# Performance work log

Measured on AMD Instinct MI355X. Metric: run time of the kernel, lower is better.

Reference implementation:

```python
import jax, jax.numpy as jnp
import numpy as np


def setup_inputs() -> dict:
    key = jax.random.key(0)
    k1, k2 = jax.random.split(key)
    x = jax.random.normal(k1, (16, 512, 64, 64), dtype=jnp.float32)
    # learned scalar (nn.Parameter init zeros; use small random value so output is nontrivial)
    gamma = jax.random.normal(k2, (1,), dtype=jnp.float32) * 0.1
    return {"x": x, "gamma": gamma}


def reference(x, gamma):
    b, c, h, w = x.shape
    q = x.reshape(b, c, h * w)                      # [b, c, hw]
    energy = jnp.einsum('bcn,bdn->bcd', q, q)       # [b, c, c]
    # reverse-max trick: max - energy, then softmax over last dim
    energy_new = jnp.max(energy, axis=-1, keepdims=True) - energy
    attention = jax.nn.softmax(energy_new, axis=-1)  # [b, c, c]
    out = jnp.einsum('bcd,bdn->bcn', attention, q).reshape(b, c, h, w)
    return gamma * out + x
```

## Files before the change

### kernel.cpp

```cpp
#include <hip/hip_runtime.h>


constexpr int Bb = 16;
constexpr int Cc = 512;
constexpr int NN = 4096;

typedef _Float16 half8 __attribute__((ext_vector_type(8)));
typedef _Float16 half4 __attribute__((ext_vector_type(4)));
typedef float float4v __attribute__((ext_vector_type(4)));

__device__ inline void gld_lds16(const _Float16* g, _Float16* l) {
    __builtin_amdgcn_global_load_lds(
        (const __attribute__((address_space(1))) unsigned int*)g,
        (__attribute__((address_space(3))) unsigned int*)l, 16, 0, 0);
}

__global__ __launch_bounds__(256) void prep_kernel(const float* __restrict__ x,
                                                   _Float16* __restrict__ Qh,
                                                   _Float16* __restrict__ QhT) {
    __shared__ float T[64][65];
    const int b = blockIdx.z;
    const int n0 = blockIdx.x * 64;
    const int d0 = blockIdx.y * 64;
    const float* xb = x + ((size_t)b * Cc + d0) * NN + n0;
    const int tid = threadIdx.x;
#pragma unroll
    for (int i = 0; i < 4; ++i) {
        int lin = tid + i * 256;
        int dr = lin >> 4;
        int c4 = (lin & 15) * 4;
        float4 v = *reinterpret_cast<const float4*>(&xb[(size_t)dr * NN + c4]);
        T[dr][c4 + 0] = v.x; T[dr][c4 + 1] = v.y;
        T[dr][c4 + 2] = v.z; T[dr][c4 + 3] = v.w;
    }
    __syncthreads();
#pragma unroll
    for (int i = 0; i < 2; ++i) {
        int widx = tid + i * 256;
        int dr = widx >> 3;
        int cn = widx & 7;
        half8 h;
#pragma unroll
        for (int j = 0; j < 8; ++j) h[j] = (_Float16)T[dr][cn * 8 + j];
        size_t dst = ((size_t)b * Cc + d0 + dr) * NN + n0 + cn * 8;
        *reinterpret_cast<half8*>(&Qh[dst]) = h;
    }
#pragma unroll
    for (int i = 0; i < 2; ++i) {
        int widx = tid + i * 256;
        int nr = widx >> 3;
        int cd = widx & 7;
        half8 h;
#pragma unroll
        for (int j = 0; j < 8; ++j) h[j] = (_Float16)T[cd * 8 + j][nr];
        size_t dst = ((size_t)b * NN + n0 + nr) * Cc + d0 + cd * 8;
        *reinterpret_cast<half8*>(&QhT[dst]) = h;
    }
}

template <int NT, int SPLIT>
__global__ __launch_bounds__(512, 4) void gram_sym(const _Float16* __restrict__ A,
                                                   float* __restrict__ D) {
    __shared__ __align__(16) float gL[128 * 129];
    _Float16* sAB = (_Float16*)gL;
    const int BPB = 10 * SPLIT;
    const int L = blockIdx.x;
    const int t0 = (L & 7) * ((BPB * Bb) >> 3) + (L >> 3);
    const int b = t0 / BPB;
    const int rem = t0 % BPB;
    const int ti = rem / SPLIT;
    const int half = rem % SPLIT;
    const int kBase = half * NT * 64;
    float* Deff = D + (size_t)half * Bb * Cc * Cc;
    int tr, tc;
    if (ti < 4)      { tr = 0; tc = ti; }
    else if (ti < 7) { tr = 1; tc = ti - 3; }
    else if (ti < 9) { tr = 2; tc = ti - 5; }
    else             { tr = 3; tc = 3; }
    const int rowTile = tr * 128;
    const int colTile = tc * 128;

    const _Float16* Ab = A + (size_t)b * Cc * NN;
    const int tid = threadIdx.x;

    float4v acc[4][2];
#pragma unroll
    for (int m = 0; m < 4; ++m)
#pragma unroll
        for (int n = 0; n < 2; ++n) acc[m][n] = (float4v){0.f, 0.f, 0.f, 0.f};

    auto stage = [&](int buf, int kt) {
        const int k0 = kBase + (kt << 6);
        _Float16* sA = sAB + buf * 8192;
        _Float16* sB = sAB + 16384 + buf * 8192;
#pragma unroll
        for (int i = 0; i < 2; ++i) {
            int idx = tid + i * 512;
            int r = idx >> 3;
            int c = idx & 7;
            int cs = (c ^ (r & 7)) << 3;
            gld_lds16(Ab + (size_t)(rowTile + r) * NN + k0 + cs, sA + idx * 8);
            gld_lds16(Ab + (size_t)(colTile + r) * NN + k0 + cs, sB + idx * 8);
        }
    };

    stage(0, 0);
    __syncthreads();

    const int wid = tid >> 6, lane = tid & 63;
    const int wr = wid >> 2, wc = wid & 3;
    const int lr = lane & 15, q = lane >> 4;

    for (int t = 0; t < NT; ++t) {
        if (t + 1 < NT) stage((t + 1) & 1, t + 1);
        const _Float16* cA = sAB + (t & 1) * 8192;
        const _Float16* cB = sAB + 16384 + (t & 1) * 8192;
#pragma unroll
        for (int s = 0; s < 2; ++s) {
            half8 af[4], bf[2];
#pragma unroll
            for (int m = 0; m < 4; ++m) {
                int r = wr * 64 + m * 16 + lr;
                int c = (s * 4 + q) ^ (r & 7);
                af[m] = *reinterpret_cast<const half8*>(&cA[r * 64 + c * 8]);
            }
#pragma unroll
            for (int n = 0; n < 2; ++n) {
                int r = wc * 32 + n * 16 + lr;
                int c = (s * 4 + q) ^ (r & 7);
                bf[n] = *reinterpret_cast<const half8*>(&cB[r * 64 + c * 8]);
            }
#pragma unroll
            for (int m = 0; m < 4; ++m)
#pragma unroll
                for (int n = 0; n < 2; ++n)
                    acc[m][n] = __builtin_amdgcn_mfma_f32_16x16x32_f16(af[m], bf[n], acc[m][n], 0, 0, 0);
        }
        __syncthreads();
    }

    __syncthreads();
#pragma unroll
    for (int m = 0; m < 4; ++m)
#pragma unroll
        for (int n = 0; n < 2; ++n)
#pragma unroll
            for (int e = 0; e < 4; ++e)
                gL[(wr * 64 + m * 16 + q * 4 + e) * 129 + wc * 32 + n * 16 + lr] = acc[m][n][e];
    __syncthreads();

    float* Db = Deff + (size_t)b * Cc * Cc;
#pragma unroll
    for (int k = 0; k < 8; ++k) {
        int c = tid + k * 512;
        int row = c >> 5;
        int col = (c & 31) << 2;
        float4 v = *reinterpret_cast<const float4*>(&gL[row * 129 + col]);
        *reinterpret_cast<float4*>(&Db[(size_t)(rowTile + row) * Cc + colTile + col]) = v;
    }
    if (tr != tc) {
#pragma unroll
        for (int k = 0; k < 8; ++k) {
            int c = tid + k * 512;
            int crow = c >> 5;
            int r4 = (c & 31) << 2;
            float4 v;
            v.x = gL[(r4 + 0) * 129 + crow];
            v.y = gL[(r4 + 1) * 129 + crow];
            v.z = gL[(r4 + 2) * 129 + crow];
            v.w = gL[(r4 + 3) * 129 + crow];
            *reinterpret_cast<float4*>(&Db[(size_t)(colTile + crow) * Cc + rowTile + r4]) = v;
        }
    }
}

template <int RES>
__global__ __launch_bounds__(512, 4) void pv_mfma(const _Float16* __restrict__ A,
                                                  const _Float16* __restrict__ Bp,
                                                  const float* __restrict__ xres,
                                                  const _Float16* __restrict__ Qh,
                                                  const float* __restrict__ gamma,
                                                  float* __restrict__ out) {
    __shared__ __align__(16) _Float16 smem[5 * 8192];
    float* L = (float*)smem;
    const int BPB = 128;
    const int Lb = blockIdx.x;
    const int t0 = (Lb & 7) * ((BPB * Bb) >> 3) + (Lb >> 3);
    const int b = t0 / BPB;
    const int rem = t0 % BPB;
    const int rowTile = (rem & 3) * 128;
    const int colTile = (rem >> 2) * 128;

    const _Float16* Ab = A + (size_t)b * Cc * Cc;
    const _Float16* Bbp = Bp + (size_t)b * NN * Cc;
    const int tid = threadIdx.x;

    float4v acc[4][2];
#pragma unroll
    for (int m = 0; m < 4; ++m)
#pragma unroll
        for (int n = 0; n < 2; ++n) acc[m][n] = (float4v){0.f, 0.f, 0.f, 0.f};

    auto stageA = [&](_Float16* dst, int kt) {
        const int k0 = kt << 6;
#pragma unroll
        for (int i = 0; i < 2; ++i) {
            int idx = tid + i * 512;
            int r = idx >> 3, c = idx & 7;
            int cs = (c ^ (r & 7)) << 3;
            gld_lds16(Ab + (size_t)(rowTile + r) * Cc + k0 + cs, dst + idx * 8);
        }
    };
    auto stageB = [&](_Float16* dst, int kt) {
        const int k0 = kt << 6;
#pragma unroll
        for (int i = 0; i < 2; ++i) {
            int idx = tid + i * 512;
            int r = idx >> 3, c = idx & 7;
            int cs = (c ^ (r & 7)) << 3;
            gld_lds16(Bbp + (size_t)(colTile + r) * Cc + k0 + cs, dst + idx * 8);
        }
    };

    _Float16* sA0 = smem;
    _Float16* sA1 = smem + 8192;
    _Float16* sB_ = smem + 16384;

    stageA(sA0, 0);
    stageB(sB_, 0);
    stageB(sB_ + 8192, 1);

    const int wid = tid >> 6, lane = tid & 63;
    const int wr = wid >> 2, wc = wid & 3;
    const int lr = lane & 15, q = lane >> 4;

#pragma unroll
    for (int t = 0; t < 8; ++t) {
        if (t < 7) asm volatile("s_waitcnt vmcnt(2)" ::: "memory");
        else       asm volatile("s_waitcnt vmcnt(0)" ::: "memory");
        __builtin_amdgcn_s_barrier();
        __builtin_amdgcn_sched_barrier(0);

        const _Float16* cA = (t & 1) ? sA1 : sA0;
        const _Float16* cB = sB_ + (t % 3) * 8192;
        half8 af[2][4], bf[2][2];
#pragma unroll
        for (int s = 0; s < 2; ++s) {
#pragma unroll
            for (int m = 0; m < 4; ++m) {
                int r = wr * 64 + m * 16 + lr;
                int c = (s * 4 + q) ^ (r & 7);
                af[s][m] = *reinterpret_cast<const half8*>(&cA[r * 64 + c * 8]);
            }
#pragma unroll
            for (int n = 0; n < 2; ++n) {
                int r = wc * 32 + n * 16 + lr;
                int c = (s * 4 + q) ^ (r & 7);
                bf[s][n] = *reinterpret_cast<const half8*>(&cB[r * 64 + c * 8]);
            }
        }
        if (t + 1 < 8) stageA((t & 1) ? sA0 : sA1, t + 1);
        if (t + 2 < 8) stageB(sB_ + ((t + 2) % 3) * 8192, t + 2);

        __builtin_amdgcn_s_setprio(1);
#pragma unroll
        for (int s = 0; s < 2; ++s)
#pragma unroll
            for (int m = 0; m < 4; ++m)
#pragma unroll
                for (int n = 0; n < 2; ++n)
                    acc[m][n] = __builtin_amdgcn_mfma_f32_16x16x32_f16(af[s][m], bf[s][n], acc[m][n], 0, 0, 0);
        __builtin_amdgcn_s_setprio(0);
    }

    __syncthreads();
#pragma unroll
    for (int m = 0; m < 4; ++m)
#pragma unroll
        for (int n = 0; n < 2; ++n)
#pragma unroll
            for (int e = 0; e < 4; ++e)
                L[(wr * 64 + m * 16 + q * 4 + e) * 129 + wc * 32 + n * 16 + lr] = acc[m][n][e];
    __syncthreads();

    const float g = gamma[0];
    const size_t base = (size_t)b * Cc * NN;
#pragma unroll
    for (int k = 0; k < 8; ++k) {
        int c = tid + k * 512;
        int row = c >> 5;
        int col = (c & 31) << 2;
        float4 v = *reinterpret_cast<const float4*>(&L[row * 129 + col]);
        size_t o = base + (size_t)(rowTile + row) * NN + colTile + col;
        float4 ov;
        if (RES == 0) {
            float4 xi = *reinterpret_cast<const float4*>(&xres[o]);
            ov.x = fmaf(g, v.x, xi.x); ov.y = fmaf(g, v.y, xi.y);
            ov.z = fmaf(g, v.z, xi.z); ov.w = fmaf(g, v.w, xi.w);
        } else {
            half4 hq = *reinterpret_cast<const half4*>(&Qh[o]);
            ov.x = fmaf(g, v.x, (float)hq[0]); ov.y = fmaf(g, v.y, (float)hq[1]);
            ov.z = fmaf(g, v.z, (float)hq[2]); ov.w = fmaf(g, v.w, (float)hq[3]);
        }
        *reinterpret_cast<float4*>(&out[o]) = ov;
    }
}

template <int HALVES>
__global__ __launch_bounds__(256) void softmax_fp16(const float* __restrict__ eA,
                                                    const float* __restrict__ eB,
                                                    _Float16* __restrict__ attH) {
    const int wave = threadIdx.x >> 6;
    const int lane = threadIdx.x & 63;
    const int row = blockIdx.x * 4 + wave;
    const float* E1 = eA + (size_t)row * Cc;
    float v[8];
    {
        float4 a = *reinterpret_cast<const float4*>(&E1[lane * 8]);
        float4 c = *reinterpret_cast<const float4*>(&E1[lane * 8 + 4]);
        v[0] = a.x; v[1] = a.y; v[2] = a.z; v[3] = a.w;
        v[4] = c.x; v[5] = c.y; v[6] = c.z; v[7] = c.w;
    }
    if (HALVES == 2) {
        const float* E2 = eB + (size_t)row * Cc;
        float4 a = *reinterpret_cast<const float4*>(&E2[lane * 8]);
        float4 c = *reinterpret_cast<const float4*>(&E2[lane * 8 + 4]);
        v[0] += a.x; v[1] += a.y; v[2] += a.z; v[3] += a.w;
        v[4] += c.x; v[5] += c.y; v[6] += c.z; v[7] += c.w;
    }
    float mn = v[0];
#pragma unroll
    for (int i = 1; i < 8; ++i) mn = fminf(mn, v[i]);
#pragma unroll
    for (int off = 32; off; off >>= 1) mn = fminf(mn, __shfl_xor(mn, off, 64));
    float sum = 0.f;
#pragma unroll
    for (int i = 0; i < 8; ++i) {
        v[i] = __expf(mn - v[i]);
        sum += v[i];
    }
#pragma unroll
    for (int off = 32; off; off >>= 1) sum += __shfl_xor(sum, off, 64);
    const float inv = 1.0f / sum;
    half8 h;
#pragma unroll
    for (int i = 0; i < 8; ++i) h[i] = (_Float16)(v[i] * inv);
    *reinterpret_cast<half8*>(&attH[(size_t)row * Cc + lane * 8]) = h;
}

#define TILE 64
#define KT 32
#define PAD 68

__global__ __launch_bounds__(256) void gram_f32(const float* __restrict__ x,
                                                float* __restrict__ energy) {
    __shared__ __align__(16) float As[KT][PAD];
    __shared__ __align__(16) float Bs[KT][PAD];
    const int b = blockIdx.z;
    const int rowTile = blockIdx.y * TILE;
    const int colTile = blockIdx.x * TILE;
    const float* Q = x + (size_t)b * Cc * NN;
    const int t = threadIdx.x;
    const int tx = t & 15;
    const int ty = t >> 4;
    float acc[4][4] = {};
    for (int k0 = 0; k0 < NN; k0 += KT) {
#pragma unroll
        for (int i = 0; i < 8; ++i) {
            int idx = t + i * 256;
            int r = idx >> 5;
            int k = idx & 31;
            As[k][r] = Q[(size_t)(rowTile + r) * NN + k0 + k];
            Bs[k][r] = Q[(size_t)(colTile + r) * NN + k0 + k];
        }
        __syncthreads();
#pragma unroll
        for (int k = 0; k < KT; ++k) {
            float4 a = *reinterpret_cast<const float4*>(&As[k][ty * 4]);
            float4 bq = *reinterpret_cast<const float4*>(&Bs[k][tx * 4]);
            float av[4] = {a.x, a.y, a.z, a.w};
            float bv[4] = {bq.x, bq.y, bq.z, bq.w};
#pragma unroll
            for (int i = 0; i < 4; ++i)
#pragma unroll
                for (int j = 0; j < 4; ++j)
                    acc[i][j] = fmaf(av[i], bv[j], acc[i][j]);
        }
        __syncthreads();
    }
    float* E = energy + (size_t)b * Cc * Cc;
#pragma unroll
    for (int i = 0; i < 4; ++i) {
        const int rowG = rowTile + ty * 4 + i;
        float4 o;
        o.x = acc[i][0]; o.y = acc[i][1]; o.z = acc[i][2]; o.w = acc[i][3];
        *reinterpret_cast<float4*>(&E[(size_t)rowG * Cc + colTile + tx * 4]) = o;
    }
}

__global__ __launch_bounds__(256) void softmax_f32(float* __restrict__ energy) {
    const int wave = threadIdx.x >> 6;
    const int lane = threadIdx.x & 63;
    const int row = blockIdx.x * 4 + wave;
    float* E = energy + (size_t)row * Cc;
    float v[8];
    float mn = 3.4e38f;
#pragma unroll
    for (int i = 0; i < 8; ++i) {
        v[i] = E[lane + 64 * i];
        mn = fminf(mn, v[i]);
    }
#pragma unroll
    for (int off = 32; off; off >>= 1) mn = fminf(mn, __shfl_xor(mn, off, 64));
    float sum = 0.f;
#pragma unroll
    for (int i = 0; i < 8; ++i) {
        v[i] = __expf(mn - v[i]);
        sum += v[i];
    }
#pragma unroll
    for (int off = 32; off; off >>= 1) sum += __shfl_xor(sum, off, 64);
    const float inv = 1.0f / sum;
#pragma unroll
    for (int i = 0; i < 8; ++i) E[lane + 64 * i] = v[i] * inv;
}

__global__ __launch_bounds__(256) void pv_f32(const float* __restrict__ x,
                                              const float* __restrict__ att,
                                              const float* __restrict__ gamma,
                                              float* __restrict__ out) {
    __shared__ __align__(16) float As[KT][PAD];
    __shared__ __align__(16) float Bs[KT][PAD];
    const int b = blockIdx.z;
    const int rowTile = blockIdx.y * TILE;
    const int colTile = blockIdx.x * TILE;
    const float* Q = x + (size_t)b * Cc * NN;
    const float* A = att + (size_t)b * Cc * Cc;
    const int t = threadIdx.x;
    const int tx = t & 15;
    const int ty = t >> 4;
    float acc[4][4] = {};
    for (int k0 = 0; k0 < Cc; k0 += KT) {
#pragma unroll
        for (int i = 0; i < 8; ++i) {
            int idx = t + i * 256;
            {
                int r = idx >> 5, k = idx & 31;
                As[k][r] = A[(size_t)(rowTile + r) * Cc + k0 + k];
            }
            {
                int k = idx >> 6, c = idx & 63;
                Bs[k][c] = Q[(size_t)(k0 + k) * NN + colTile + c];
            }
        }
        __syncthreads();
#pragma unroll
        for (int k = 0; k < KT; ++k) {
            float4 a = *reinterpret_cast<const float4*>(&As[k][ty * 4]);
            float4 bq = *reinterpret_cast<const float4*>(&Bs[k][tx * 4]);
            float av[4] = {a.x, a.y, a.z, a.w};
            float bv[4] = {bq.x, bq.y, bq.z, bq.w};
#pragma unroll
            for (int i = 0; i < 4; ++i)
#pragma unroll
                for (int j = 0; j < 4; ++j)
                    acc[i][j] = fmaf(av[i], bv[j], acc[i][j]);
        }
        __syncthreads();
    }
    const float g = gamma[0];
#pragma unroll
    for (int i = 0; i < 4; ++i) {
        const int rowG = rowTile + ty * 4 + i;
        const size_t base = (size_t)rowG * NN + colTile + tx * 4;
        const float4 xi = *reinterpret_cast<const float4*>(&Q[base]);
        float4 o;
        o.x = fmaf(g, acc[i][0], xi.x);
        o.y = fmaf(g, acc[i][1], xi.y);
        o.z = fmaf(g, acc[i][2], xi.z);
        o.w = fmaf(g, acc[i][3], xi.w);
        *reinterpret_cast<float4*>(&out[(size_t)b * Cc * NN + base]) = o;
    }
}

extern "C" void kernel_launch(void* const* d_in, const int* in_sizes, int n_in,
                              void* d_out, int out_size, void* d_ws, size_t ws_size,
                              hipStream_t stream) {
    const float* x = (const float*)d_in[0];
    const float* gamma = (const float*)d_in[1];
    float* out = (float*)d_out;

    const size_t NQ = (size_t)Bb * Cc * NN;
    const size_t NE = (size_t)Bb * Cc * Cc;
    const size_t NEED1 = NQ * 2 * 2 + NE * 4 + NE * 2;
    const size_t NEED2 = NQ * 2 * 2 + NE * 4 * 2;
    const size_t NEED3 = NQ * 2 * 2 + NE * 4 * 2 + NE * 2;

    if (ws_size >= NEED3) {
        _Float16* Qh = (_Float16*)d_ws;
        _Float16* QhT = Qh + NQ;
        float* eA = (float*)(QhT + NQ);
        _Float16* attH = (_Float16*)(eA + 2 * NE);

        prep_kernel<<<dim3(NN / 64, Cc / 64, Bb), 256, 0, stream>>>(x, Qh, QhT);
        gram_sym<32, 2><<<dim3(20 * Bb), 512, 0, stream>>>(Qh, eA);
        softmax_fp16<2><<<dim3(Bb * Cc / 4), 256, 0, stream>>>(eA, eA + NE, attH);
        pv_mfma<1><<<dim3(128 * Bb), 512, 0, stream>>>(attH, QhT, x, Qh, gamma, out);
    } else if (ws_size >= NEED2) {
        _Float16* Qh = (_Float16*)d_ws;
        _Float16* QhT = Qh + NQ;
        float* eA = (float*)(QhT + NQ);
        _Float16* attH = Qh;

        prep_kernel<<<dim3(NN / 64, Cc / 64, Bb), 256, 0, stream>>>(x, Qh, QhT);
        gram_sym<32, 2><<<dim3(20 * Bb), 512, 0, stream>>>(Qh, eA);
        softmax_fp16<2><<<dim3(Bb * Cc / 4), 256, 0, stream>>>(eA, eA + NE, attH);
        pv_mfma<0><<<dim3(128 * Bb), 512, 0, stream>>>(attH, QhT, x, nullptr, gamma, out);
    } else if (ws_size >= NEED1) {
        _Float16* Qh = (_Float16*)d_ws;
        _Float16* QhT = Qh + NQ;
        float* energy = (float*)(QhT + NQ);
        _Float16* attH = (_Float16*)(energy + NE);

        prep_kernel<<<dim3(NN / 64, Cc / 64, Bb), 256, 0, stream>>>(x, Qh, QhT);
        gram_sym<64, 1><<<dim3(10 * Bb), 512, 0, stream>>>(Qh, energy);
        softmax_fp16<1><<<dim3(Bb * Cc / 4), 256, 0, stream>>>(energy, nullptr, attH);
        pv_mfma<1><<<dim3(128 * Bb), 512, 0, stream>>>(attH, QhT, x, Qh, gamma, out);
    } else {
        float* energy = (float*)d_ws;
        gram_f32<<<dim3(Cc / TILE, Cc / TILE, Bb), 256, 0, stream>>>(x, energy);
        softmax_f32<<<dim3(Bb * Cc / 4), 256, 0, stream>>>(energy);
        pv_f32<<<dim3(NN / TILE, Cc / TILE, Bb), 256, 0, stream>>>(x, energy, gamma, out);
    }
}
```

Measured before the change: 165.1 us.

## Halve K-tile and LDS footprint, split gram into four K-slices for occupancy

The gram and PV kernels now stage 32-wide K tiles instead of 64-wide, with a new XOR swizzle and half-size LDS buffers. The epilogue is written back in two 64-row halves so the staging buffer fits in the smaller LDS allocation. Launch bounds rise to 8 blocks per CU, and when workspace allows, the gram kernel splits K four ways to get 640 blocks instead of 320, with softmax summing four partial energies. This trades more barriers, more loop iterations and extra partial-energy traffic for higher occupancy and better CU fill.

```diff
diff --git a/kernel.cpp b/kernel.cpp
--- a/kernel.cpp
+++ b/kernel.cpp
@@ -58,10 +58,11 @@
     }
 }
 
-template <int NT, int SPLIT>
-__global__ __launch_bounds__(512, 4) void gram_sym(const _Float16* __restrict__ A,
+template <int SPLIT>
+__global__ __launch_bounds__(512, 8) void gram_sym(const _Float16* __restrict__ A,
                                                    float* __restrict__ D) {
-    __shared__ __align__(16) float gL[128 * 129];
+    constexpr int NT = 128 / SPLIT;
+    __shared__ __align__(16) float gL[64 * 132];
     _Float16* sAB = (_Float16*)gL;
     const int BPB = 10 * SPLIT;
     const int L = blockIdx.x;
@@ -70,7 +71,7 @@
     const int rem = t0 % BPB;
     const int ti = rem / SPLIT;
     const int half = rem % SPLIT;
-    const int kBase = half * NT * 64;
+    const int kBase = half * NT * 32;
     float* Deff = D + (size_t)half * Bb * Cc * Cc;
     int tr, tc;
     if (ti < 4)      { tr = 0; tc = ti; }
@@ -90,18 +91,13 @@
         for (int n = 0; n < 2; ++n) acc[m][n] = (float4v){0.f, 0.f, 0.f, 0.f};
 
     auto stage = [&](int buf, int kt) {
-        const int k0 = kBase + (kt << 6);
-        _Float16* sA = sAB + buf * 8192;
-        _Float16* sB = sAB + 16384 + buf * 8192;
-#pragma unroll
-        for (int i = 0; i < 2; ++i) {
-            int idx = tid + i * 512;
-            int r = idx >> 3;
-            int c = idx & 7;
-            int cs = (c ^ (r & 7)) << 3;
-            gld_lds16(Ab + (size_t)(rowTile + r) * NN + k0 + cs, sA + idx * 8);
-            gld_lds16(Ab + (size_t)(colTile + r) * NN + k0 + cs, sB + idx * 8);
-        }
+        const int k0 = kBase + (kt << 5);
+        _Float16* sA = sAB + buf * 4096;
+        _Float16* sB = sAB + 8192 + buf * 4096;
+        int r = tid >> 2, c = tid & 3;
+        int cs = (c ^ ((r >> 1) & 3)) << 3;
+        gld_lds16(Ab + (size_t)(rowTile + r) * NN + k0 + cs, sA + tid * 8);
+        gld_lds16(Ab + (size_t)(colTile + r) * NN + k0 + cs, sB + tid * 8);
     };
 
     stage(0, 0);
@@ -113,75 +109,78 @@
 
     for (int t = 0; t < NT; ++t) {
         if (t + 1 < NT) stage((t + 1) & 1, t + 1);
-        const _Float16* cA = sAB + (t & 1) * 8192;
-        const _Float16* cB = sAB + 16384 + (t & 1) * 8192;
-#pragma unroll
-        for (int s = 0; s < 2; ++s) {
-            half8 af[4], bf[2];
-#pragma unroll
-            for (int m = 0; m < 4; ++m) {
-                int r = wr * 64 + m * 16 + lr;
-                int c = (s * 4 + q) ^ (r & 7);
-                af[m] = *reinterpret_cast<const half8*>(&cA[r * 64 + c * 8]);
+        const _Float16* cA = sAB + (t & 1) * 4096;
+        const _Float16* cB = sAB + 8192 + (t & 1) * 4096;
+        half8 af[4], bf[2];
+#pragma unroll
+        for (int m = 0; m < 4; ++m) {
+            int r = wr * 64 + m * 16 + lr;
+            int c = q ^ ((r >> 1) & 3);
+            af[m] = *reinterpret_cast<const half8*>(&cA[r * 32 + c * 8]);
+        }
+#pragma unroll
+        for (int n = 0; n < 2; ++n) {
+            int r = wc * 32 + n * 16 + lr;
+            int c = q ^ ((r >> 1) & 3);
+            bf[n] = *reinterpret_cast<const half8*>(&cB[r * 32 + c * 8]);
+        }
+        __builtin_amdgcn_s_setprio(1);
+#pragma unroll
+        for (int m = 0; m < 4; ++m)
+#pragma unroll
+            for (int n = 0; n < 2; ++n)
+                acc[m][n] = __builtin_amdgcn_mfma_f32_16x16x32_f16(af[m], bf[n], acc[m][n], 0, 0, 0);
+        __builtin_amdgcn_s_setprio(0);
+        __syncthreads();
+    }
+
+    float* Db = Deff + (size_t)b * Cc * Cc;
+#pragma unroll
+    for (int h = 0; h < 2; ++h) {
+        __syncthreads();
+        if (wr == h) {
+#pragma unroll
+            for (int m = 0; m < 4; ++m)
+#pragma unroll
+                for (int n = 0; n < 2; ++n)
+#pragma unroll
+                    for (int e = 0; e < 4; ++e)
+                        gL[(m * 16 + q * 4 + e) * 132 + wc * 32 + n * 16 + lr] = acc[m][n][e];
+        }
+        __syncthreads();
+#pragma unroll
+        for (int k = 0; k < 4; ++k) {
+            int c2 = tid + k * 512;
+            int row = c2 >> 5;
+            int col = (c2 & 31) << 2;
+            float4 v = *reinterpret_cast<const float4*>(&gL[row * 132 + col]);
+            *reinterpret_cast<float4*>(&Db[(size_t)(rowTile + h * 64 + row) * Cc + colTile + col]) = v;
+        }
+        if (tr != tc) {
+#pragma unroll
+            for (int k = 0; k < 4; ++k) {
+                int c2 = tid + k * 512;
+                int crow = c2 >> 4;
+                int r4 = (c2 & 15) << 2;
+                float4 v;
+                v.x = gL[(r4 + 0) * 132 + crow];
+                v.y = gL[(r4 + 1) * 132 + crow];
+                v.z = gL[(r4 + 2) * 132 + crow];
+                v.w = gL[(r4 + 3) * 132 + crow];
+                *reinterpret_cast<float4*>(&Db[(size_t)(colTile + crow) * Cc + rowTile + h * 64 + r4]) = v;
             }
-#pragma unroll
-            for (int n = 0; n < 2; ++n) {
-                int r = wc * 32 + n * 16 + lr;
-                int c = (s * 4 + q) ^ (r & 7);
-                bf[n] = *reinterpret_cast<const half8*>(&cB[r * 64 + c * 8]);
-            }
-#pragma unroll
-            for (int m = 0; m < 4; ++m)
-#pragma unroll
-                for (int n = 0; n < 2; ++n)
-                    acc[m][n] = __builtin_amdgcn_mfma_f32_16x16x32_f16(af[m], bf[n], acc[m][n], 0, 0, 0);
-        }
-        __syncthreads();
-    }
-
-    __syncthreads();
-#pragma unroll
-    for (int m = 0; m < 4; ++m)
-#pragma unroll
-        for (int n = 0; n < 2; ++n)
-#pragma unroll
-            for (int e = 0; e < 4; ++e)
-                gL[(wr * 64 + m * 16 + q * 4 + e) * 129 + wc * 32 + n * 16 + lr] = acc[m][n][e];
-    __syncthreads();
-
-    float* Db = Deff + (size_t)b * Cc * Cc;
-#pragma unroll
-    for (int k = 0; k < 8; ++k) {
-        int c = tid + k * 512;
-        int row = c >> 5;
-        int col = (c & 31) << 2;
-        float4 v = *reinterpret_cast<const float4*>(&gL[row * 129 + col]);
-        *reinterpret_cast<float4*>(&Db[(size_t)(rowTile + row) * Cc + colTile + col]) = v;
-    }
-    if (tr != tc) {
-#pragma unroll
-        for (int k = 0; k < 8; ++k) {
-            int c = tid + k * 512;
-            int crow = c >> 5;
-            int r4 = (c & 31) << 2;
-            float4 v;
-            v.x = gL[(r4 + 0) * 129 + crow];
-            v.y = gL[(r4 + 1) * 129 + crow];
-            v.z = gL[(r4 + 2) * 129 + crow];
-            v.w = gL[(r4 + 3) * 129 + crow];
-            *reinterpret_cast<float4*>(&Db[(size_t)(colTile + crow) * Cc + rowTile + r4]) = v;
         }
     }
 }
 
 template <int RES>
-__global__ __launch_bounds__(512, 4) void pv_mfma(const _Float16* __restrict__ A,
+__global__ __launch_bounds__(512, 8) void pv_mfma(const _Float16* __restrict__ A,
                                                   const _Float16* __restrict__ Bp,
                                                   const float* __restrict__ xres,
                                                   const _Float16* __restrict__ Qh,
                                                   const float* __restrict__ gamma,
                                                   float* __restrict__ out) {
-    __shared__ __align__(16) _Float16 smem[5 * 8192];
+    __shared__ __align__(16) _Float16 smem[5 * 4096];
     float* L = (float*)smem;
     const int BPB = 128;
     const int Lb = blockIdx.x;
@@ -202,127 +201,119 @@
         for (int n = 0; n < 2; ++n) acc[m][n] = (float4v){0.f, 0.f, 0.f, 0.f};
 
     auto stageA = [&](_Float16* dst, int kt) {
-        const int k0 = kt << 6;
-#pragma unroll
-        for (int i = 0; i < 2; ++i) {
-            int idx = tid + i * 512;
-            int r = idx >> 3, c = idx & 7;
-            int cs = (c ^ (r & 7)) << 3;
-            gld_lds16(Ab + (size_t)(rowTile + r) * Cc + k0 + cs, dst + idx * 8);
-        }
+        const int k0 = kt << 5;
+        int r = tid >> 2, c = tid & 3;
+        int cs = (c ^ ((r >> 1) & 3)) << 3;
+        gld_lds16(Ab + (size_t)(rowTile + r) * Cc + k0 + cs, dst + tid * 8);
     };
     auto stageB = [&](_Float16* dst, int kt) {
-        const int k0 = kt << 6;
-#pragma unroll
-        for (int i = 0; i < 2; ++i) {
-            int idx = tid + i * 512;
-            int r = idx >> 3, c = idx & 7;
-            int cs = (c ^ (r & 7)) << 3;
-            gld_lds16(Bbp + (size_t)(colTile + r) * Cc + k0 + cs, dst + idx * 8);
-        }
+        const int k0 = kt << 5;
+        int r = tid >> 2, c = tid & 3;
+        int cs = (c ^ ((r >> 1) & 3)) << 3;
+        gld_lds16(Bbp + (size_t)(colTile + r) * Cc + k0 + cs, dst + tid * 8);
     };
 
     _Float16* sA0 = smem;
-    _Float16* sA1 = smem + 8192;
-    _Float16* sB_ = smem + 16384;
+    _Float16* sA1 = smem + 4096;
+    _Float16* sB_ = smem + 8192;
 
     stageA(sA0, 0);
     stageB(sB_, 0);
-    stageB(sB_ + 8192, 1);
+    stageB(sB_ + 4096, 1);
 
     const int wid = tid >> 6, lane = tid & 63;
     const int wr = wid >> 2, wc = wid & 3;
     const int lr = lane & 15, q = lane >> 4;
 
 #pragma unroll
-    for (int t = 0; t < 8; ++t) {
-        if (t < 7) asm volatile("s_waitcnt vmcnt(2)" ::: "memory");
-        else       asm volatile("s_waitcnt vmcnt(0)" ::: "memory");
+    for (int t = 0; t < 16; ++t) {
+        if (t < 15) asm volatile("s_waitcnt vmcnt(1)" ::: "memory");
+        else        asm volatile("s_waitcnt vmcnt(0)" ::: "memory");
         __builtin_amdgcn_s_barrier();
         __builtin_amdgcn_sched_barrier(0);
 
         const _Float16* cA = (t & 1) ? sA1 : sA0;
-        const _Float16* cB = sB_ + (t % 3) * 8192;
-        half8 af[2][4], bf[2][2];
-#pragma unroll
-        for (int s = 0; s < 2; ++s) {
-#pragma unroll
-            for (int m = 0; m < 4; ++m) {
-                int r = wr * 64 + m * 16 + lr;
-                int c = (s * 4 + q) ^ (r & 7);
-                af[s][m] = *reinterpret_cast<const half8*>(&cA[r * 64 + c * 8]);
-            }
-#pragma unroll
-            for (int n = 0; n < 2; ++n) {
-                int r = wc * 32 + n * 16 + lr;
-                int c = (s * 4 + q) ^ (r & 7);
-                bf[s][n] = *reinterpret_cast<const half8*>(&cB[r * 64 + c * 8]);
-            }
-        }
-        if (t + 1 < 8) stageA((t & 1) ? sA0 : sA1, t + 1);
-        if (t + 2 < 8) stageB(sB_ + ((t + 2) % 3) * 8192, t + 2);
+        const _Float16* cB = sB_ + (t % 3) * 4096;
+        half8 af[4], bf[2];
+#pragma unroll
+        for (int m = 0; m < 4; ++m) {
+            int r = wr * 64 + m * 16 + lr;
+            int c = q ^ ((r >> 1) & 3);
+            af[m] = *reinterpret_cast<const half8*>(&cA[r * 32 + c * 8]);
+        }
+#pragma unroll
+        for (int n = 0; n < 2; ++n) {
+            int r = wc * 32 + n * 16 + lr;
+            int c = q ^ ((r >> 1) & 3);
+            bf[n] = *reinterpret_cast<const half8*>(&cB[r * 32 + c * 8]);
+        }
+        if (t + 1 < 16) stageA((t & 1) ? sA0 : sA1, t + 1);
+        if (t + 2 < 16) stageB(sB_ + ((t + 2) % 3) * 4096, t + 2);
 
         __builtin_amdgcn_s_setprio(1);
 #pragma unroll
-        for (int s = 0; s < 2; ++s)
-#pragma unroll
-            for (int m = 0; m < 4; ++m)
-#pragma unroll
-                for (int n = 0; n < 2; ++n)
-                    acc[m][n] = __builtin_amdgcn_mfma_f32_16x16x32_f16(af[s][m], bf[s][n], acc[m][n], 0, 0, 0);
+        for (int m = 0; m < 4; ++m)
+#pragma unroll
+            for (int n = 0; n < 2; ++n)
+                acc[m][n] = __builtin_amdgcn_mfma_f32_16x16x32_f16(af[m], bf[n], acc[m][n], 0, 0, 0);
         __builtin_amdgcn_s_setprio(0);
     }
-
-    __syncthreads();
-#pragma unroll
-    for (int m = 0; m < 4; ++m)
-#pragma unroll
-        for (int n = 0; n < 2; ++n)
-#pragma unroll
-            for (int e = 0; e < 4; ++e)
-                L[(wr * 64 + m * 16 + q * 4 + e) * 129 + wc * 32 + n * 16 + lr] = acc[m][n][e];
-    __syncthreads();
 
     const float g = gamma[0];
     const size_t base = (size_t)b * Cc * NN;
 #pragma unroll
-    for (int k = 0; k < 8; ++k) {
-        int c = tid + k * 512;
-        int row = c >> 5;
-        int col = (c & 31) << 2;
-        float4 v = *reinterpret_cast<const float4*>(&L[row * 129 + col]);
-        size_t o = base + (size_t)(rowTile + row) * NN + colTile + col;
-        float4 ov;
-        if (RES == 0) {
-            float4 xi = *reinterpret_cast<const float4*>(&xres[o]);
-            ov.x = fmaf(g, v.x, xi.x); ov.y = fmaf(g, v.y, xi.y);
-            ov.z = fmaf(g, v.z, xi.z); ov.w = fmaf(g, v.w, xi.w);
-        } else {
-            half4 hq = *reinterpret_cast<const half4*>(&Qh[o]);
-            ov.x = fmaf(g, v.x, (float)hq[0]); ov.y = fmaf(g, v.y, (float)hq[1]);
-            ov.z = fmaf(g, v.z, (float)hq[2]); ov.w = fmaf(g, v.w, (float)hq[3]);
-        }
-        *reinterpret_cast<float4*>(&out[o]) = ov;
+    for (int h = 0; h < 2; ++h) {
+        __syncthreads();
+        if (wr == h) {
+#pragma unroll
+            for (int m = 0; m < 4; ++m)
+#pragma unroll
+                for (int n = 0; n < 2; ++n)
+#pragma unroll
+                    for (int e = 0; e < 4; ++e)
+                        L[(m * 16 + q * 4 + e) * 132 + wc * 32 + n * 16 + lr] = acc[m][n][e];
+        }
+        __syncthreads();
+#pragma unroll
+        for (int k = 0; k < 4; ++k) {
+            int c2 = tid + k * 512;
+            int row = c2 >> 5;
+            int col = (c2 & 31) << 2;
+            float4 v = *reinterpret_cast<const float4*>(&L[row * 132 + col]);
+            size_t o = base + (size_t)(rowTile + h * 64 + row) * NN + colTile + col;
+            float4 ov;
+            if (RES == 0) {
+                float4 xi = *reinterpret_cast<const float4*>(&xres[o]);
+                ov.x = fmaf(g, v.x, xi.x); ov.y = fmaf(g, v.y, xi.y);
+                ov.z = fmaf(g, v.z, xi.z); ov.w = fmaf(g, v.w, xi.w);
+            } else {
+                half4 hq = *reinterpret_cast<const half4*>(&Qh[o]);
+                ov.x = fmaf(g, v.x, (float)hq[0]); ov.y = fmaf(g, v.y, (float)hq[1]);
+                ov.z = fmaf(g, v.z, (float)hq[2]); ov.w = fmaf(g, v.w, (float)hq[3]);
+            }
+            *reinterpret_cast<float4*>(&out[o]) = ov;
+        }
     }
 }
 
 template <int HALVES>
 __global__ __launch_bounds__(256) void softmax_fp16(const float* __restrict__ eA,
-                                                    const float* __restrict__ eB,
                                                     _Float16* __restrict__ attH) {
+    const size_t NE = (size_t)Bb * Cc * Cc;
     const int wave = threadIdx.x >> 6;
     const int lane = threadIdx.x & 63;
     const int row = blockIdx.x * 4 + wave;
-    const float* E1 = eA + (size_t)row * Cc;
     float v[8];
     {
+        const float* E1 = eA + (size_t)row * Cc;
         float4 a = *reinterpret_cast<const float4*>(&E1[lane * 8]);
         float4 c = *reinterpret_cast<const float4*>(&E1[lane * 8 + 4]);
         v[0] = a.x; v[1] = a.y; v[2] = a.z; v[3] = a.w;
         v[4] = c.x; v[5] = c.y; v[6] = c.z; v[7] = c.w;
     }
-    if (HALVES == 2) {
-        const float* E2 = eB + (size_t)row * Cc;
+#pragma unroll
+    for (int p = 1; p < HALVES; ++p) {
+        const float* E2 = eA + p * NE + (size_t)row * Cc;
         float4 a = *reinterpret_cast<const float4*>(&E2[lane * 8]);
         float4 c = *reinterpret_cast<const float4*>(&E2[lane * 8 + 4]);
         v[0] += a.x; v[1] += a.y; v[2] += a.z; v[3] += a.w;
@@ -492,40 +483,33 @@
 
     const size_t NQ = (size_t)Bb * Cc * NN;
     const size_t NE = (size_t)Bb * Cc * Cc;
-    const size_t NEED1 = NQ * 2 * 2 + NE * 4 + NE * 2;
-    const size_t NEED2 = NQ * 2 * 2 + NE * 4 * 2;
-    const size_t NEED3 = NQ * 2 * 2 + NE * 4 * 2 + NE * 2;
-
-    if (ws_size >= NEED3) {
+    const size_t NEED1 = NQ * 4 + NE * 4 + NE * 2;
+    const size_t NEED2 = NQ * 4 + NE * 8 + NE * 2;
+    const size_t NEED4 = NQ * 4 + NE * 16 + NE * 2;
+
+    if (ws_size >= NEED1) {
         _Float16* Qh = (_Float16*)d_ws;
         _Float16* QhT = Qh + NQ;
         float* eA = (float*)(QhT + NQ);
-        _Float16* attH = (_Float16*)(eA + 2 * NE);
-
-        prep_kernel<<<dim3(NN / 64, Cc / 64, Bb), 256, 0, stream>>>(x, Qh, QhT);
-        gram_sym<32, 2><<<dim3(20 * Bb), 512, 0, stream>>>(Qh, eA);
-        softmax_fp16<2><<<dim3(Bb * Cc / 4), 256, 0, stream>>>(eA, eA + NE, attH);
-        pv_mfma<1><<<dim3(128 * Bb), 512, 0, stream>>>(attH, QhT, x, Qh, gamma, out);
-    } else if (ws_size >= NEED2) {
-        _Float16* Qh = (_Float16*)d_ws;
-        _Float16* QhT = Qh + NQ;
-        float* eA = (float*)(QhT + NQ);
-        _Float16* attH = Qh;
-
-        prep_kernel<<<dim3(NN / 64, Cc / 64, Bb), 256, 0, stream>>>(x, Qh, QhT);
-        gram_sym<32, 2><<<dim3(20 * Bb), 512, 0, stream>>>(Qh, eA);
-        softmax_fp16<2><<<dim3(Bb * Cc / 4), 256, 0, stream>>>(eA, eA + NE, attH);
-        pv_mfma<0><<<dim3(128 * Bb), 512, 0, stream>>>(attH, QhT, x, nullptr, gamma, out);
-    } else if (ws_size >= NEED1) {
-        _Float16* Qh = (_Float16*)d_ws;
-        _Float16* QhT = Qh + NQ;
-        float* energy = (float*)(QhT + NQ);
-        _Float16* attH = (_Float16*)(energy + NE);
-
-        prep_kernel<<<dim3(NN / 64, Cc / 64, Bb), 256, 0, stream>>>(x, Qh, QhT);
-        gram_sym<64, 1><<<dim3(10 * Bb), 512, 0, stream>>>(Qh, energy);
-        softmax_fp16<1><<<dim3(Bb * Cc / 4), 256, 0, stream>>>(energy, nullptr, attH);
-        pv_mfma<1><<<dim3(128 * Bb), 512, 0, stream>>>(attH, QhT, x, Qh, gamma, out);
+        if (ws_size >= NEED4) {
+            _Float16* attH = (_Float16*)(eA + 4 * NE);
+            prep_kernel<<<dim3(NN / 64, Cc / 64, Bb), 256, 0, stream>>>(x, Qh, QhT);
+            gram_sym<4><<<dim3(40 * Bb), 512, 0, stream>>>(Qh, eA);
+            softmax_fp16<4><<<dim3(Bb * Cc / 4), 256, 0, stream>>>(eA, attH);
+            pv_mfma<1><<<dim3(128 * Bb), 512, 0, stream>>>(attH, QhT, x, Qh, gamma, out);
+        } else if (ws_size >= NEED2) {
+            _Float16* attH = (_Float16*)(eA + 2 * NE);
+            prep_kernel<<<dim3(NN / 64, Cc / 64, Bb), 256, 0, stream>>>(x, Qh, QhT);
+            gram_sym<2><<<dim3(20 * Bb), 512, 0, stream>>>(Qh, eA);
+            softmax_fp16<2><<<dim3(Bb * Cc / 4), 256, 0, stream>>>(eA, attH);
+            pv_mfma<1><<<dim3(128 * Bb), 512, 0, stream>>>(attH, QhT, x, Qh, gamma, out);
+        } else {
+            _Float16* attH = (_Float16*)(eA + NE);
+            prep_kernel<<<dim3(NN / 64, Cc / 64, Bb), 256, 0, stream>>>(x, Qh, QhT);
+            gram_sym<1><<<dim3(10 * Bb), 512, 0, stream>>>(Qh, eA);
+            softmax_fp16<1><<<dim3(Bb * Cc / 4), 256, 0, stream>>>(eA, attH);
+            pv_mfma<1><<<dim3(128 * Bb), 512, 0, stream>>>(attH, QhT, x, Qh, gamma, out);
+        }
     } else {
         float* energy = (float*)d_ws;
         gram_f32<<<dim3(Cc / TILE, Cc / TILE, Bb), 256, 0, stream>>>(x, energy);
```

Measured after the change: 199.1 us. 20.5% more time.

## Halve pv_mfma LDS footprint with K=32 stages and split epilogue to raise occupancy

Applied to the files above, without the earlier changes.

The PV GEMM kernel now stages 32-wide K slices instead of 64, which halves the A/B LDS buffers, and the swizzle is adapted to 4 chunks per row. The epilogue writes the accumulator tile to LDS in two 64-row halves, so the staging area fits in the smaller shared allocation. Launch bounds are raised to 6 blocks per CU to exploit the lower LDS use. In exchange there are twice as many barrier-synchronised iterations with fewer MFMAs each, plus an extra barrier pair in the epilogue.

```diff
diff --git a/kernel.cpp b/kernel.cpp
--- a/kernel.cpp
+++ b/kernel.cpp
@@ -175,13 +175,13 @@
 }
 
 template <int RES>
-__global__ __launch_bounds__(512, 4) void pv_mfma(const _Float16* __restrict__ A,
+__global__ __launch_bounds__(512, 6) void pv_mfma(const _Float16* __restrict__ A,
                                                   const _Float16* __restrict__ Bp,
                                                   const float* __restrict__ xres,
                                                   const _Float16* __restrict__ Qh,
                                                   const float* __restrict__ gamma,
                                                   float* __restrict__ out) {
-    __shared__ __align__(16) _Float16 smem[5 * 8192];
+    __shared__ __align__(16) _Float16 smem[5 * 4096];
     float* L = (float*)smem;
     const int BPB = 128;
     const int Lb = blockIdx.x;
@@ -202,107 +202,98 @@
         for (int n = 0; n < 2; ++n) acc[m][n] = (float4v){0.f, 0.f, 0.f, 0.f};
 
     auto stageA = [&](_Float16* dst, int kt) {
-        const int k0 = kt << 6;
-#pragma unroll
-        for (int i = 0; i < 2; ++i) {
-            int idx = tid + i * 512;
-            int r = idx >> 3, c = idx & 7;
-            int cs = (c ^ (r & 7)) << 3;
-            gld_lds16(Ab + (size_t)(rowTile + r) * Cc + k0 + cs, dst + idx * 8);
-        }
+        const int k0 = kt << 5;
+        int r = tid >> 2, c = tid & 3;
+        int cs = (c ^ ((r >> 1) & 3)) << 3;
+        gld_lds16(Ab + (size_t)(rowTile + r) * Cc + k0 + cs, dst + tid * 8);
     };
     auto stageB = [&](_Float16* dst, int kt) {
-        const int k0 = kt << 6;
-#pragma unroll
-        for (int i = 0; i < 2; ++i) {
-            int idx = tid + i * 512;
-            int r = idx >> 3, c = idx & 7;
-            int cs = (c ^ (r & 7)) << 3;
-            gld_lds16(Bbp + (size_t)(colTile + r) * Cc + k0 + cs, dst + idx * 8);
-        }
+        const int k0 = kt << 5;
+        int r = tid >> 2, c = tid & 3;
+        int cs = (c ^ ((r >> 1) & 3)) << 3;
+        gld_lds16(Bbp + (size_t)(colTile + r) * Cc + k0 + cs, dst + tid * 8);
     };
 
     _Float16* sA0 = smem;
-    _Float16* sA1 = smem + 8192;
-    _Float16* sB_ = smem + 16384;
+    _Float16* sA1 = smem + 4096;
+    _Float16* sB_ = smem + 8192;
 
     stageA(sA0, 0);
     stageB(sB_, 0);
-    stageB(sB_ + 8192, 1);
+    stageB(sB_ + 4096, 1);
 
     const int wid = tid >> 6, lane = tid & 63;
     const int wr = wid >> 2, wc = wid & 3;
     const int lr = lane & 15, q = lane >> 4;
 
 #pragma unroll
-    for (int t = 0; t < 8; ++t) {
-        if (t < 7) asm volatile("s_waitcnt vmcnt(2)" ::: "memory");
-        else       asm volatile("s_waitcnt vmcnt(0)" ::: "memory");
+    for (int t = 0; t < 16; ++t) {
+        if (t < 15) asm volatile("s_waitcnt vmcnt(1)" ::: "memory");
+        else        asm volatile("s_waitcnt vmcnt(0)" ::: "memory");
         __builtin_amdgcn_s_barrier();
         __builtin_amdgcn_sched_barrier(0);
 
         const _Float16* cA = (t & 1) ? sA1 : sA0;
-        const _Float16* cB = sB_ + (t % 3) * 8192;
-        half8 af[2][4], bf[2][2];
-#pragma unroll
-        for (int s = 0; s < 2; ++s) {
-#pragma unroll
-            for (int m = 0; m < 4; ++m) {
-                int r = wr * 64 + m * 16 + lr;
-                int c = (s * 4 + q) ^ (r & 7);
-                af[s][m] = *reinterpret_cast<const half8*>(&cA[r * 64 + c * 8]);
-            }
-#pragma unroll
-            for (int n = 0; n < 2; ++n) {
-                int r = wc * 32 + n * 16 + lr;
-                int c = (s * 4 + q) ^ (r & 7);
-                bf[s][n] = *reinterpret_cast<const half8*>(&cB[r * 64 + c * 8]);
-            }
-        }
-        if (t + 1 < 8) stageA((t & 1) ? sA0 : sA1, t + 1);
-        if (t + 2 < 8) stageB(sB_ + ((t + 2) % 3) * 8192, t + 2);
+        const _Float16* cB = sB_ + (t % 3) * 4096;
+        half8 af[4], bf[2];
+#pragma unroll
+        for (int m = 0; m < 4; ++m) {
+            int r = wr * 64 + m * 16 + lr;
+            int c = q ^ ((r >> 1) & 3);
+            af[m] = *reinterpret_cast<const half8*>(&cA[r * 32 + c * 8]);
+        }
+#pragma unroll
+        for (int n = 0; n < 2; ++n) {
+            int r = wc * 32 + n * 16 + lr;
+            int c = q ^ ((r >> 1) & 3);
+            bf[n] = *reinterpret_cast<const half8*>(&cB[r * 32 + c * 8]);
+        }
+        if (t + 1 < 16) stageA((t & 1) ? sA0 : sA1, t + 1);
+        if (t + 2 < 16) stageB(sB_ + ((t + 2) % 3) * 4096, t + 2);
 
         __builtin_amdgcn_s_setprio(1);
 #pragma unroll
-        for (int s = 0; s < 2; ++s)
-#pragma unroll
-            for (int m = 0; m < 4; ++m)
-#pragma unroll
-                for (int n = 0; n < 2; ++n)
-                    acc[m][n] = __builtin_amdgcn_mfma_f32_16x16x32_f16(af[s][m], bf[s][n], acc[m][n], 0, 0, 0);
+        for (int m = 0; m < 4; ++m)
+#pragma unroll
+            for (int n = 0; n < 2; ++n)
+                acc[m][n] = __builtin_amdgcn_mfma_f32_16x16x32_f16(af[m], bf[n], acc[m][n], 0, 0, 0);
         __builtin_amdgcn_s_setprio(0);
     }
-
-    __syncthreads();
-#pragma unroll
-    for (int m = 0; m < 4; ++m)
-#pragma unroll
-        for (int n = 0; n < 2; ++n)
-#pragma unroll
-            for (int e = 0; e < 4; ++e)
-                L[(wr * 64 + m * 16 + q * 4 + e) * 129 + wc * 32 + n * 16 + lr] = acc[m][n][e];
-    __syncthreads();
 
     const float g = gamma[0];
     const size_t base = (size_t)b * Cc * NN;
 #pragma unroll
-    for (int k = 0; k < 8; ++k) {
-        int c = tid + k * 512;
-        int row = c >> 5;
-        int col = (c & 31) << 2;
-        float4 v = *reinterpret_cast<const float4*>(&L[row * 129 + col]);
-        size_t o = base + (size_t)(rowTile + row) * NN + colTile + col;
-        float4 ov;
-        if (RES == 0) {
-            float4 xi = *reinterpret_cast<const float4*>(&xres[o]);
-            ov.x = fmaf(g, v.x, xi.x); ov.y = fmaf(g, v.y, xi.y);
-            ov.z = fmaf(g, v.z, xi.z); ov.w = fmaf(g, v.w, xi.w);
-        } else {
-            half4 hq = *reinterpret_cast<const half4*>(&Qh[o]);
-            ov.x = fmaf(g, v.x, (float)hq[0]); ov.y = fmaf(g, v.y, (float)hq[1]);
-            ov.z = fmaf(g, v.z, (float)hq[2]); ov.w = fmaf(g, v.w, (float)hq[3]);
-        }
-        *reinterpret_cast<float4*>(&out[o]) = ov;
+    for (int h = 0; h < 2; ++h) {
+        __syncthreads();
+        if (wr == h) {
+#pragma unroll
+            for (int m = 0; m < 4; ++m)
+#pragma unroll
+                for (int n = 0; n < 2; ++n)
+#pragma unroll
+                    for (int e = 0; e < 4; ++e)
+                        L[(m * 16 + q * 4 + e) * 132 + wc * 32 + n * 16 + lr] = acc[m][n][e];
+        }
+        __syncthreads();
+#pragma unroll
+        for (int k = 0; k < 4; ++k) {
+            int c2 = tid + k * 512;
+            int row = c2 >> 5;
+            int col = (c2 & 31) << 2;
+            float4 v = *reinterpret_cast<const float4*>(&L[row * 132 + col]);
+            size_t o = base + (size_t)(rowTile + h * 64 + row) * NN + colTile + col;
+            float4 ov;
+            if (RES == 0) {
+                float4 xi = *reinterpret_cast<const float4*>(&xres[o]);
+                ov.x = fmaf(g, v.x, xi.x); ov.y = fmaf(g, v.y, xi.y);
+                ov.z = fmaf(g, v.z, xi.z); ov.w = fmaf(g, v.w, xi.w);
+            } else {
+                half4 hq = *reinterpret_cast<const half4*>(&Qh[o]);
+                ov.x = fmaf(g, v.x, (float)hq[0]); ov.y = fmaf(g, v.y, (float)hq[1]);
+                ov.z = fmaf(g, v.z, (float)hq[2]); ov.w = fmaf(g, v.w, (float)hq[3]);
+            }
+            *reinterpret_cast<float4*>(&out[o]) = ov;
+        }
     }
 }
 
```

Result: no change. 166.3 us (+0.7%).
